# Optimization experiments

Hardware: AMD Instinct MI355X
Metric: run time of the kernel (lower is better)

Reference implementation:

```python
import jax, jax.numpy as jnp
import numpy as np


def setup_inputs() -> dict:
    key = jax.random.key(0)
    k1, k2, k3, k4 = jax.random.split(key, 4)
    B, T, E, H = 16, 2048, 1024, 128
    x = jax.random.normal(k1, (B, T, E), dtype=jnp.float32)
    Wk = jax.random.normal(k2, (E, H), dtype=jnp.float32) * (E ** -0.5)
    Wq = jax.random.normal(k3, (E, H), dtype=jnp.float32) * (E ** -0.5)
    Wv = jax.random.normal(k4, (E, H), dtype=jnp.float32) * (E ** -0.5)
    return {"x": x, "Wk": Wk, "Wq": Wq, "Wv": Wv}


def reference(x, Wk, Wq, Wv):
    # x: [B,T,E]; Wk/Wq/Wv: [E,H]
    B, T, E = x.shape
    H = Wk.shape[1]
    k = jnp.einsum('bte,eh->bth', x, Wk)
    q = jnp.einsum('bte,eh->bth', x, Wq)
    v = jnp.einsum('bte,eh->bth', x, Wv)
    # scores [B,T,T]; original masks with -inf THEN scales (equivalent math)
    scores = jnp.einsum('bqh,bkh->bqk', q, k) * (H ** -0.5)
    causal = jnp.tril(jnp.ones((T, T), dtype=bool))
    scores = jnp.where(causal, scores, -jnp.inf)
    weights = jax.nn.softmax(scores, axis=-1)
    # dropout disabled (eval mode reference)
    return jnp.einsum('bqk,bkh->bqh', weights, v)
```

## Files before the change

kernel.cpp:

```cpp
#include <hip/hip_runtime.h>

#define B_ 16
#define T_ 2048
#define E_ 1024
#define H_ 128

typedef short bf16x8 __attribute__((ext_vector_type(8)));
typedef float f32x4 __attribute__((ext_vector_type(4)));
typedef unsigned short u16x4 __attribute__((ext_vector_type(4)));

static __device__ __forceinline__ unsigned short f2bf(float f) {
    unsigned int u = __float_as_uint(f);
    u += 0x7FFFu + ((u >> 16) & 1u);
    return (unsigned short)(u >> 16);
}
static __device__ __forceinline__ unsigned int pk2(unsigned short a, unsigned short b) {
    return (unsigned int)a | ((unsigned int)b << 16);
}
static __device__ __forceinline__ bf16x8 frag(uint4 v) {
    return __builtin_bit_cast(bf16x8, v);
}
static __device__ __forceinline__ void gl16(const unsigned short* g, unsigned short* l) {
    __builtin_amdgcn_global_load_lds(
        (const __attribute__((address_space(1))) void*)g,
        (__attribute__((address_space(3))) void*)l, 16, 0, 0);
}

__global__ __launch_bounds__(256) void cvtw_kernel(
    const float* __restrict__ w0, const float* __restrict__ w1,
    const float* __restrict__ w2, unsigned short* __restrict__ wt)
{
    int g   = blockIdx.x * 256 + threadIdx.x;
    int arr = g >> 14;
    int rem = g & 16383;
    int h   = rem >> 7;
    int e0  = (rem & 127) * 8;
    const float* src = (arr == 0) ? w0 : (arr == 1) ? w1 : w2;
    unsigned short b[8];
#pragma unroll
    for (int i = 0; i < 8; i++) b[i] = f2bf(src[(size_t)(e0 + i) * H_ + h]);
    uint4 o;
    o.x = pk2(b[0], b[1]); o.y = pk2(b[2], b[3]);
    o.z = pk2(b[4], b[5]); o.w = pk2(b[6], b[7]);
    *(uint4*)&wt[(size_t)(arr * 128 + h) * E_ + e0] = o;
}

__global__ __launch_bounds__(256, 4) void proj_kernel(
    const float* __restrict__ x,
    const unsigned short* __restrict__ wt,
    unsigned short* __restrict__ q_ws,
    unsigned short* __restrict__ kp_ws,
    unsigned short* __restrict__ vt_ws)
{
    const int m0 = blockIdx.x * 64;
    const int c0 = blockIdx.y * 192;
    __shared__ __align__(16) unsigned short As[2][64 * 32];
    __shared__ __align__(16) unsigned short Bs[2][192 * 32];

    const int tid  = threadIdx.x;
    const int lane = tid & 63;
    const int w    = tid >> 6;
    const int quad = lane >> 4;
    const int lm   = lane & 15;
    const int wc   = w * 48;

    const int arow = tid >> 2;
    const int acol = (tid & 3) * 8;
    const float* gx = x + (size_t)(m0 + arow) * E_ + acol;

    const unsigned short* gw = wt + (size_t)(c0 + (tid >> 2)) * E_ + (tid & 3) * 8;

    const f32x4 z4 = {0.f, 0.f, 0.f, 0.f};
    f32x4 acc[4][3];
#pragma unroll
    for (int i = 0; i < 4; i++)
#pragma unroll
        for (int j = 0; j < 3; j++) acc[i][j] = z4;

    auto stageB = [&](int kb, int buf) {
        const unsigned short* g = gw + kb * 32;
        unsigned short* l = &Bs[buf][tid * 8];
        gl16(g,                    l);
        gl16(g + (size_t)64  * E_, l + 2048);
        gl16(g + (size_t)128 * E_, l + 4096);
    };
    auto writeA = [&](float4 v0, float4 v1, int buf) {
        uint4 o;
        o.x = pk2(f2bf(v0.x), f2bf(v0.y));
        o.y = pk2(f2bf(v0.z), f2bf(v0.w));
        o.z = pk2(f2bf(v1.x), f2bf(v1.y));
        o.w = pk2(f2bf(v1.z), f2bf(v1.w));
        *(uint4*)&As[buf][arow * 32 + acol] = o;
    };

    float4 a0 = *(const float4*)gx;
    float4 a1 = *(const float4*)(gx + 4);
    stageB(0, 0);
    writeA(a0, a1, 0);
    a0 = *(const float4*)(gx + 32);
    a1 = *(const float4*)(gx + 36);

    for (int kb = 0; kb < 32; kb++) {
        const int cb = kb & 1;
        __syncthreads();

        const int kb2 = (kb + 2 < 32) ? kb + 2 : 31;
        float4 n0 = *(const float4*)(gx + kb2 * 32);
        float4 n1 = *(const float4*)(gx + kb2 * 32 + 4);
        if (kb + 1 < 32) {
            stageB(kb + 1, cb ^ 1);
            writeA(a0, a1, cb ^ 1);
        }

        bf16x8 af[4], bf[3];
#pragma unroll
        for (int am = 0; am < 4; am++)
            af[am] = frag(*(const uint4*)&As[cb][(am * 16 + lm) * 32 + quad * 8]);
#pragma unroll
        for (int bn = 0; bn < 3; bn++)
            bf[bn] = frag(*(const uint4*)&Bs[cb][(wc + bn * 16 + lm) * 32 + quad * 8]);
#pragma unroll
        for (int am = 0; am < 4; am++)
#pragma unroll
            for (int bn = 0; bn < 3; bn++)
                acc[am][bn] = __builtin_amdgcn_mfma_f32_16x16x32_bf16(
                    af[am], bf[bn], acc[am][bn], 0, 0, 0);

        a0 = n0; a1 = n1;
    }

#pragma unroll
    for (int am = 0; am < 4; am++)
#pragma unroll
        for (int bn = 0; bn < 3; bn++) {
            const int gcol  = c0 + wc + bn * 16 + lm;
            const int sel   = gcol >> 7;
            const int c     = gcol & 127;
            const int rbase = m0 + am * 16 + quad * 4;
            const int bb    = rbase >> 11;
            const int t     = rbase & 2047;
            if (sel == 0) {
#pragma unroll
                for (int r = 0; r < 4; r++)
                    q_ws[(size_t)(rbase + r) * H_ + c] = f2bf(acc[am][bn][r]);
            } else if (sel == 1) {
#pragma unroll
                for (int r = 0; r < 4; r++) {
                    int tt = t + r;
                    kp_ws[(size_t)(bb * 64 + (tt >> 5)) * 4096 +
                          (c >> 5) * 1024 + (tt & 31) * 32 + (c & 31)] =
                        f2bf(acc[am][bn][r]);
                }
            } else {
                u16x4 pv;
#pragma unroll
                for (int r = 0; r < 4; r++) pv[r] = f2bf(acc[am][bn][r]);
                *(u16x4*)&vt_ws[((size_t)(bb * 64 + (t >> 5)) * 128 + c) * 32 + (t & 31)] = pv;
            }
        }
}

__global__ __launch_bounds__(256, 2) void attn_kernel(
    const unsigned short* __restrict__ q_ws,
    const unsigned short* __restrict__ kp_ws,
    const unsigned short* __restrict__ vt_ws,
    float* __restrict__ out)
{
    __shared__ __align__(16) unsigned short Ks[3][4096];
    __shared__ __align__(16) unsigned short Vs[3][4096];
    __shared__ __align__(16) unsigned short Ps[4][16][40];

    const int bid   = blockIdx.x;
    const int batch = bid & 15;
    const int p     = (bid >> 4) & 15;
    const int tau   = (bid >> 8) ? (31 - p) : p;
    const int nkt   = 2 * tau + 2;

    const int tid  = threadIdx.x;
    const int lane = tid & 63;
    const int ww   = tid >> 6;
    const int quad = lane >> 4;
    const int lm   = lane & 15;
    const float scale = 0.08838834764831845f;

    bf16x8 ones;
#pragma unroll
    for (int i = 0; i < 8; i++) ones[i] = (short)0x3F80;
    const f32x4 z4 = {0.f, 0.f, 0.f, 0.f};

    const size_t bq = (size_t)batch * T_ * H_;
    const int so = ww * 1024 + lane * 8;
    const unsigned short* Kt = kp_ws + (size_t)(batch * 64) * 4096 + so;
    const unsigned short* Vt = vt_ws + (size_t)(batch * 64) * 4096 + so;

    auto stage = [&](int t, int b) {
        const unsigned short* kg = Kt + (size_t)t * 4096;
        const unsigned short* vg = Vt + (size_t)t * 4096;
        gl16(kg,       &Ks[b][ww * 1024]);
        gl16(kg + 512, &Ks[b][ww * 1024 + 512]);
        gl16(vg,       &Vs[b][ww * 1024]);
        gl16(vg + 512, &Vs[b][ww * 1024 + 512]);
    };

    bf16x8 qf[4];
#pragma unroll
    for (int h = 0; h < 4; h++)
        qf[h] = frag(*(const uint4*)(q_ws + bq +
                 (size_t)(tau * 64 + ww * 16 + lm) * H_ + h * 32 + quad * 8));

    f32x4 o[9];
#pragma unroll
    for (int f = 0; f < 9; f++) o[f] = z4;

    stage(0, 0);
    stage(1, 1);

    for (int kt = 0; kt < nkt; kt++) {
        const int cb = kt % 3;
        asm volatile("s_waitcnt vmcnt(4) lgkmcnt(0)" ::: "memory");
        __builtin_amdgcn_sched_barrier(0);
        __builtin_amdgcn_s_barrier();
        __builtin_amdgcn_sched_barrier(0);

        int ks = kt + 2; if (ks > nkt - 1) ks = nkt - 1;
        stage(ks, (kt + 2) % 3);

        f32x4 st0 = z4, st1 = z4;
        __builtin_amdgcn_s_setprio(1);
#pragma unroll
        for (int h = 0; h < 4; h++) {
            bf16x8 kf0 = frag(*(const uint4*)&Ks[cb][(h * 32 + lm) * 32 + quad * 8]);
            bf16x8 kf1 = frag(*(const uint4*)&Ks[cb][(h * 32 + 16 + lm) * 32 + quad * 8]);
            st0 = __builtin_amdgcn_mfma_f32_16x16x32_bf16(kf0, qf[h], st0, 0, 0, 0);
            st1 = __builtin_amdgcn_mfma_f32_16x16x32_bf16(kf1, qf[h], st1, 0, 0, 0);
        }
        __builtin_amdgcn_s_setprio(0);

        const int qg = tau * 64 + ww * 16 + lm;
        const int k0 = kt * 32;
        u16x4 pa, pb;
#pragma unroll
        for (int r = 0; r < 4; r++) {
            int kv0 = k0 + quad * 4 + r;
            float e0 = __expf(st0[r] * scale);
            float e1 = __expf(st1[r] * scale);
            pa[r] = (kv0      <= qg) ? f2bf(e0) : (unsigned short)0;
            pb[r] = (kv0 + 16 <= qg) ? f2bf(e1) : (unsigned short)0;
        }
        *(u16x4*)&Ps[ww][lm][quad * 4]      = pa;
        *(u16x4*)&Ps[ww][lm][16 + quad * 4] = pb;
        bf16x8 pf = frag(*(const uint4*)&Ps[ww][lm][quad * 8]);

        __builtin_amdgcn_s_setprio(1);
#pragma unroll
        for (int f = 0; f < 8; f++) {
            bf16x8 vfr = frag(*(const uint4*)&Vs[cb][(f * 16 + lm) * 32 + quad * 8]);
            o[f] = __builtin_amdgcn_mfma_f32_16x16x32_bf16(pf, vfr, o[f], 0, 0, 0);
        }
        o[8] = __builtin_amdgcn_mfma_f32_16x16x32_bf16(pf, ones, o[8], 0, 0, 0);
        __builtin_amdgcn_s_setprio(0);
    }

    float* op = out + bq + (size_t)(tau * 64 + ww * 16) * H_;
#pragma unroll
    for (int r = 0; r < 4; r++) {
        float inv = 1.f / o[8][r];
#pragma unroll
        for (int f = 0; f < 8; f++)
            op[(size_t)(quad * 4 + r) * H_ + f * 16 + lm] = o[f][r] * inv;
    }
}

extern "C" void kernel_launch(void* const* d_in, const int* in_sizes, int n_in,
                              void* d_out, int out_size, void* d_ws, size_t ws_size,
                              hipStream_t stream)
{
    const float* x  = (const float*)d_in[0];
    const float* Wk = (const float*)d_in[1];
    const float* Wq = (const float*)d_in[2];
    const float* Wv = (const float*)d_in[3];
    float* out = (float*)d_out;

    const size_t MH = (size_t)B_ * T_ * H_;
    unsigned short* q_ws  = (unsigned short*)d_ws;
    unsigned short* kp_ws = q_ws + MH;
    unsigned short* vt_ws = kp_ws + MH;
    unsigned short* wt    = vt_ws + MH;

    cvtw_kernel<<<dim3(192), dim3(256), 0, stream>>>(Wq, Wk, Wv, wt);
    proj_kernel<<<dim3(512, 2), dim3(256), 0, stream>>>(x, wt, q_ws, kp_ws, vt_ws);
    attn_kernel<<<dim3(512), dim3(256), 0, stream>>>(q_ws, kp_ws, vt_ws, out);
}
```

Before: 292.4 us.

## Deepen projection GEMM pipeline with triple-buffered B and manual waitcnt barriers

Reworks the projection kernel's K-loop into a deeper software pipeline. The B tile (weights, loaded asynchronously into LDS) gets a third buffer. A ring of three register slots prefetches x several iterations ahead. A hand-written s_waitcnt vmcnt(5) with an explicit s_barrier replaces __syncthreads, the loop is fully unrolled, and s_setprio raises priority around the MFMA block. The goal is to hide global-load latency behind matrix math, at the cost of more LDS and registers, which is why the launch-bounds occupancy hint drops from 4 to 3. The vmcnt count is fragile and must exactly match the number of in-flight loads.

```diff
diff --git a/kernel.cpp b/kernel.cpp
--- a/kernel.cpp
+++ b/kernel.cpp
@@ -45,7 +45,7 @@
     *(uint4*)&wt[(size_t)(arr * 128 + h) * E_ + e0] = o;
 }
 
-__global__ __launch_bounds__(256, 4) void proj_kernel(
+__global__ __launch_bounds__(256, 3) void proj_kernel(
     const float* __restrict__ x,
     const unsigned short* __restrict__ wt,
     unsigned short* __restrict__ q_ws,
@@ -55,7 +55,7 @@
     const int m0 = blockIdx.x * 64;
     const int c0 = blockIdx.y * 192;
     __shared__ __align__(16) unsigned short As[2][64 * 32];
-    __shared__ __align__(16) unsigned short Bs[2][192 * 32];
+    __shared__ __align__(16) unsigned short Bs[3][192 * 32];
 
     const int tid  = threadIdx.x;
     const int lane = tid & 63;
@@ -84,49 +84,56 @@
         gl16(g + (size_t)64  * E_, l + 2048);
         gl16(g + (size_t)128 * E_, l + 4096);
     };
-    auto writeA = [&](float4 v0, float4 v1, int buf) {
+
+    float4 ar0[3], ar1[3];
+    auto ldA = [&](int kb, int slot) {
+        ar0[slot] = *(const float4*)(gx + kb * 32);
+        ar1[slot] = *(const float4*)(gx + kb * 32 + 4);
+    };
+    auto writeA = [&](int slot, int buf) {
         uint4 o;
-        o.x = pk2(f2bf(v0.x), f2bf(v0.y));
-        o.y = pk2(f2bf(v0.z), f2bf(v0.w));
-        o.z = pk2(f2bf(v1.x), f2bf(v1.y));
-        o.w = pk2(f2bf(v1.z), f2bf(v1.w));
+        o.x = pk2(f2bf(ar0[slot].x), f2bf(ar0[slot].y));
+        o.y = pk2(f2bf(ar0[slot].z), f2bf(ar0[slot].w));
+        o.z = pk2(f2bf(ar1[slot].x), f2bf(ar1[slot].y));
+        o.w = pk2(f2bf(ar1[slot].z), f2bf(ar1[slot].w));
         *(uint4*)&As[buf][arow * 32 + acol] = o;
     };
 
-    float4 a0 = *(const float4*)gx;
-    float4 a1 = *(const float4*)(gx + 4);
+    ldA(0, 0);
     stageB(0, 0);
-    writeA(a0, a1, 0);
-    a0 = *(const float4*)(gx + 32);
-    a1 = *(const float4*)(gx + 36);
-
+    ldA(1, 1);
+    ldA(2, 2);
+    stageB(1, 1);
+    writeA(0, 0);
+
+#pragma unroll
     for (int kb = 0; kb < 32; kb++) {
-        const int cb = kb & 1;
-        __syncthreads();
-
-        const int kb2 = (kb + 2 < 32) ? kb + 2 : 31;
-        float4 n0 = *(const float4*)(gx + kb2 * 32);
-        float4 n1 = *(const float4*)(gx + kb2 * 32 + 4);
-        if (kb + 1 < 32) {
-            stageB(kb + 1, cb ^ 1);
-            writeA(a0, a1, cb ^ 1);
-        }
+        asm volatile("s_waitcnt vmcnt(5) lgkmcnt(0)" ::: "memory");
+        __builtin_amdgcn_sched_barrier(0);
+        __builtin_amdgcn_s_barrier();
+        __builtin_amdgcn_sched_barrier(0);
+
+        if (kb + 1 < 32) writeA((kb + 1) % 3, (kb + 1) & 1);
+
+        ldA((kb + 3 < 32) ? kb + 3 : 31, kb % 3);
+        stageB((kb + 2 < 32) ? kb + 2 : 31, (kb + 2) % 3);
 
         bf16x8 af[4], bf[3];
 #pragma unroll
         for (int am = 0; am < 4; am++)
-            af[am] = frag(*(const uint4*)&As[cb][(am * 16 + lm) * 32 + quad * 8]);
+            af[am] = frag(*(const uint4*)&As[kb & 1][(am * 16 + lm) * 32 + quad * 8]);
 #pragma unroll
         for (int bn = 0; bn < 3; bn++)
-            bf[bn] = frag(*(const uint4*)&Bs[cb][(wc + bn * 16 + lm) * 32 + quad * 8]);
+            bf[bn] = frag(*(const uint4*)&Bs[kb % 3][(wc + bn * 16 + lm) * 32 + quad * 8]);
+
+        __builtin_amdgcn_s_setprio(1);
 #pragma unroll
         for (int am = 0; am < 4; am++)
 #pragma unroll
             for (int bn = 0; bn < 3; bn++)
                 acc[am][bn] = __builtin_amdgcn_mfma_f32_16x16x32_bf16(
                     af[am], bf[bn], acc[am][bn], 0, 0, 0);
-
-        a0 = n0; a1 = n1;
+        __builtin_amdgcn_s_setprio(0);
     }
 
 #pragma unroll
```

Result: slower. 306.2 us (+4.7%).
